# Kernel optimization log

Hardware: AMD Instinct MI355X
Metric: run time of the kernel (lower is better)

The kernel has to match this reference:

```python
import jax, jax.numpy as jnp
import numpy as np

GX, GY = 480, 360  # grid_size
EPS = 1e-5  # BatchNorm eps


def _bn(x, g, b):
    # BatchNorm1d in training mode: batch statistics, biased variance
    m = jnp.mean(x, axis=0)
    v = jnp.var(x, axis=0)
    return (x - m) * jax.lax.rsqrt(v + EPS) * g + b


def setup_inputs() -> dict:
    key = jax.random.key(0)
    ks = jax.random.split(key, 16)
    B, N, F = 2, 200000, 9
    pt_fea = jax.random.normal(ks[0], (B, N, F), dtype=jnp.float32)
    xy_ind = jax.random.randint(ks[1], (B, N, 2), 0, 360, dtype=jnp.int64)

    def lin(k, fi, fo):
        s = 1.0 / np.sqrt(fi)
        kw, kb = jax.random.split(k)
        W = jax.random.uniform(kw, (fi, fo), jnp.float32, -s, s)
        b = jax.random.uniform(kb, (fo,), jnp.float32, -s, s)
        return W, b

    W1, b1 = lin(ks[2], F, 64)
    W2, b2 = lin(ks[3], 64, 128)
    W3, b3 = lin(ks[4], 128, 256)
    W4, b4 = lin(ks[5], 256, 64)
    return {
        "pt_fea": pt_fea, "xy_ind": xy_ind,
        "bn0_g": jnp.ones((F,)), "bn0_b": jnp.zeros((F,)),
        "W1": W1, "b1": b1, "bn1_g": jnp.ones((64,)), "bn1_b": jnp.zeros((64,)),
        "W2": W2, "b2": b2, "bn2_g": jnp.ones((128,)), "bn2_b": jnp.zeros((128,)),
        "W3": W3, "b3": b3, "bn3_g": jnp.ones((256,)), "bn3_b": jnp.zeros((256,)),
        "W4": W4, "b4": b4,
    }


def reference(pt_fea, xy_ind, bn0_g, bn0_b, W1, b1, bn1_g, bn1_b,
              W2, b2, bn2_g, bn2_b, W3, b3, bn3_g, bn3_b, W4, b4):
    B, N, F = pt_fea.shape
    P = B * N  # total points
    x = pt_fea.reshape(P, F)

    # composite voxel key = batch * GX*GY + ix * GY + iy (equivalent to
    # torch.unique over the padded [batch, ix, iy] rows)
    bidx = jnp.repeat(jnp.arange(B, dtype=xy_ind.dtype), N)
    ind = xy_ind.reshape(P, 2)
    keys = bidx * (GX * GY) + ind[:, 0] * GY + ind[:, 1]
    unq_keys, unq_inv = jnp.unique(keys, return_inverse=True, size=P, fill_value=-1)

    # per-point MLP (BN -> Lin -> BN -> ReLU -> ... )
    h = _bn(x, bn0_g, bn0_b)
    h = jax.nn.relu(_bn(h @ W1 + b1, bn1_g, bn1_b))
    h = jax.nn.relu(_bn(h @ W2 + b2, bn2_g, bn2_b))
    h = jax.nn.relu(_bn(h @ W3 + b3, bn3_g, bn3_b))
    h = h @ W4 + b4  # [P, 64]

    # scatter_mean over voxel segments
    sums = jax.ops.segment_sum(h, unq_inv, num_segments=P)
    cnt = jax.ops.segment_sum(jnp.ones((P,), h.dtype), unq_inv, num_segments=P)
    pooled = sums / jnp.maximum(cnt, 1.0)[:, None]

    # decode unique keys back to [batch, ix, iy]; padded slots have key=-1
    ub = unq_keys // (GX * GY)
    rem = unq_keys % (GX * GY)
    unq = jnp.stack([ub, rem // GY, rem % GY], axis=1).astype(jnp.int64)
    return unq, pooled
```

## Files before the change

kernel.cpp:

```cpp
#include <hip/hip_runtime.h>
#include <hip/hip_bf16.h>

#define GXGY 172800
#define GYC  360
#define NKEYS 345600
#define SCAN_NB 338
#define STATS_NBLK 256
#define SQOFF 65536

typedef short short8_t __attribute__((ext_vector_type(8)));
typedef float floatx4 __attribute__((ext_vector_type(4)));

__device__ inline float bf2f(unsigned short u) {
  union { unsigned int i; float f; } v;
  v.i = ((unsigned int)u) << 16;
  return v.f;
}
__device__ inline unsigned short f2bf(float f) {
  union { float f; unsigned int i; } v;
  v.f = f;
  unsigned int lsb = (v.i >> 16) & 1u;
  return (unsigned short)((v.i + 0x7FFFu + lsb) >> 16);
}
__device__ inline unsigned int pk2bf(float lo, float hi) {
  __hip_bfloat162 h = __float22bfloat162_rn(float2{lo, hi});
  union { __hip_bfloat162 h; unsigned int u; } c;
  c.h = h;
  return c.u;
}
__device__ inline unsigned int aff2(unsigned int pr, float a0, float c0, float a1, float c1) {
  union { unsigned int i; float f; } t0, t1;
  t0.i = pr << 16; t1.i = pr & 0xFFFF0000u;
  float v0 = fmaxf(fmaf(t0.f, a0, c0), 0.f);
  float v1 = fmaxf(fmaf(t1.f, a1, c1), 0.f);
  return pk2bf(v0, v1);
}

__global__ __launch_bounds__(1024) void k_detect(const int* __restrict__ xy, int* __restrict__ flag) {
  __shared__ int any;
  if (threadIdx.x == 0) any = 0;
  __syncthreads();
  if (xy[threadIdx.x * 2 + 1] != 0) atomicOr(&any, 1);
  __syncthreads();
  if (threadIdx.x == 0) *flag = any;
}

__device__ inline void load_xy(const int* xy, const int* flag, int p, int& ix, int& iy) {
  if (*flag) { ix = xy[(size_t)p * 2]; iy = xy[(size_t)p * 2 + 1]; }
  else       { ix = xy[(size_t)p * 4]; iy = xy[(size_t)p * 4 + 2]; }
}


__global__ __launch_bounds__(256) void k_count(const int* __restrict__ xy, const int* __restrict__ flag,
                                               int* __restrict__ counts, int P, int N) {
  int p = blockIdx.x * 256 + threadIdx.x;
  if (p >= P) return;
  int ix, iy;
  load_xy(xy, flag, p, ix, iy);
  int key = ((p >= N) ? GXGY : 0) + ix * GYC + iy;
  atomicAdd(&counts[key], 1);
}

__global__ __launch_bounds__(256) void k_scan1(const int* __restrict__ counts, int* __restrict__ prefix,
                                               int* __restrict__ blockTot) {
  __shared__ int ssum[256];
  int base = blockIdx.x * 1024;
  int f[4];
  int tsum = 0;
#pragma unroll
  for (int i = 0; i < 4; ++i) {
    int k = base + threadIdx.x * 4 + i;
    f[i] = (k < NKEYS && counts[k] > 0) ? 1 : 0;
    tsum += f[i];
  }
  ssum[threadIdx.x] = tsum;
  __syncthreads();
  for (int off = 1; off < 256; off <<= 1) {
    int v = (threadIdx.x >= off) ? ssum[threadIdx.x - off] : 0;
    __syncthreads();
    if (threadIdx.x >= off) ssum[threadIdx.x] += v;
    __syncthreads();
  }
  int run = (threadIdx.x == 0) ? 0 : ssum[threadIdx.x - 1];
#pragma unroll
  for (int i = 0; i < 4; ++i) {
    int k = base + threadIdx.x * 4 + i;
    if (k < NKEYS) prefix[k] = run;
    run += f[i];
  }
  if (threadIdx.x == 255) blockTot[blockIdx.x] = ssum[255];
}

__global__ __launch_bounds__(256) void k_scan1v(const int* __restrict__ counts, int* __restrict__ prefixS,
                                                int* __restrict__ blockTot) {
  __shared__ int ssum[256];
  int base = blockIdx.x * 1024;
  int f[4];
  int tsum = 0;
#pragma unroll
  for (int i = 0; i < 4; ++i) {
    int k = base + threadIdx.x * 4 + i;
    f[i] = (k < NKEYS) ? counts[k] : 0;
    tsum += f[i];
  }
  ssum[threadIdx.x] = tsum;
  __syncthreads();
  for (int off = 1; off < 256; off <<= 1) {
    int v = (threadIdx.x >= off) ? ssum[threadIdx.x - off] : 0;
    __syncthreads();
    if (threadIdx.x >= off) ssum[threadIdx.x] += v;
    __syncthreads();
  }
  int run = (threadIdx.x == 0) ? 0 : ssum[threadIdx.x - 1];
#pragma unroll
  for (int i = 0; i < 4; ++i) {
    int k = base + threadIdx.x * 4 + i;
    if (k < NKEYS) prefixS[k] = run;
    run += f[i];
  }
  if (threadIdx.x == 255) blockTot[blockIdx.x] = ssum[255];
}

__global__ __launch_bounds__(512) void k_scan2(const int* __restrict__ blockTot, int* __restrict__ blockOff,
                                               int* __restrict__ dU) {
  __shared__ int s[512];
  int v = (threadIdx.x < SCAN_NB) ? blockTot[threadIdx.x] : 0;
  s[threadIdx.x] = v;
  __syncthreads();
  for (int off = 1; off < 512; off <<= 1) {
    int t = (threadIdx.x >= off) ? s[threadIdx.x - off] : 0;
    __syncthreads();
    if (threadIdx.x >= off) s[threadIdx.x] += t;
    __syncthreads();
  }
  if (threadIdx.x < SCAN_NB) blockOff[threadIdx.x] = s[threadIdx.x] - v;
  if (threadIdx.x == 511) *dU = s[511];
}

__global__ __launch_bounds__(256) void k_fillunq(const int* __restrict__ counts, const int* __restrict__ prefix,
                                                 const int* __restrict__ blockOff,
                                                 const int* __restrict__ prefixS, const int* __restrict__ blockOffS,
                                                 float* __restrict__ out_unq,
                                                 int2* __restrict__ rankCS) {
  int k = blockIdx.x * 256 + threadIdx.x;
  if (k >= NKEYS) return;
  int cnt = counts[k];
  if (cnt <= 0) return;
  int r = prefix[k] + blockOff[k >> 10];
  rankCS[r] = make_int2(cnt, prefixS[k] + blockOffS[k >> 10]);
  int b = k / GXGY;
  int rem = k % GXGY;
  out_unq[(size_t)r * 3 + 0] = (float)b;
  out_unq[(size_t)r * 3 + 1] = (float)(rem / GYC);
  out_unq[(size_t)r * 3 + 2] = (float)(rem % GYC);
}

__global__ __launch_bounds__(256) void k_pad(float* __restrict__ out_unq, const int* __restrict__ dU, int P) {
  int r = blockIdx.x * 256 + threadIdx.x;
  if (r >= P) return;
  if (r >= *dU) {
    out_unq[(size_t)r * 3 + 0] = -1.f;
    out_unq[(size_t)r * 3 + 1] = 479.f;
    out_unq[(size_t)r * 3 + 2] = 359.f;
  }
}

__global__ __launch_bounds__(256) void k_sortpts(const int* __restrict__ xy, const int* __restrict__ flag,
                                                 const int* __restrict__ prefixS,
                                                 const int* __restrict__ blockOffS, int* __restrict__ cursor,
                                                 int* __restrict__ sorted, int P, int N) {
  int p = blockIdx.x * 256 + threadIdx.x;
  if (p >= P) return;
  int ix, iy;
  load_xy(xy, flag, p, ix, iy);
  int key = ((p >= N) ? GXGY : 0) + ix * GYC + iy;
  int slot = prefixS[key] + blockOffS[key >> 10] + atomicAdd(&cursor[key], 1);
  sorted[slot] = p;
}


__global__ __launch_bounds__(256) void k_stats9(const float* __restrict__ x, int P, float* __restrict__ partials) {
  float s[9] = {0}, q[9] = {0};
  for (int p = blockIdx.x * 256 + threadIdx.x; p < P; p += STATS_NBLK * 256) {
#pragma unroll
    for (int k = 0; k < 9; ++k) {
      float v = x[(size_t)p * 9 + k];
      s[k] += v;
      q[k] += v * v;
    }
  }
  __shared__ float ls[256 * 9];
#pragma unroll
  for (int k = 0; k < 9; ++k) ls[threadIdx.x * 9 + k] = s[k];
  __syncthreads();
  if (threadIdx.x < 9) {
    float acc = 0;
    for (int t = 0; t < 256; ++t) acc += ls[t * 9 + threadIdx.x];
    partials[blockIdx.x * 9 + threadIdx.x] = acc;
  }
  __syncthreads();
#pragma unroll
  for (int k = 0; k < 9; ++k) ls[threadIdx.x * 9 + k] = q[k];
  __syncthreads();
  if (threadIdx.x < 9) {
    float acc = 0;
    for (int t = 0; t < 256; ++t) acc += ls[t * 9 + threadIdx.x];
    partials[SQOFF + blockIdx.x * 9 + threadIdx.x] = acc;
  }
}

__global__ void k_finalize(const float* __restrict__ partials, const float* __restrict__ gam,
                           const float* __restrict__ bet, float* __restrict__ ac, int F, int P) {
  int f = threadIdx.x;
  if (f >= F) return;
  float s = 0.f, q = 0.f;
  for (int blk = 0; blk < STATS_NBLK; ++blk) {
    s += partials[blk * F + f];
    q += partials[SQOFF + blk * F + f];
  }
  float mean = s / (float)P;
  float var = q / (float)P - mean * mean;
  float A = gam[f] * rsqrtf(var + 1e-5f);
  ac[f] = A;
  ac[256 + f] = bet[f] - mean * A;
}

__global__ void k_finalize_at(const float* __restrict__ stats, const float* __restrict__ gam,
                              const float* __restrict__ bet, float* __restrict__ ac, int F, int P) {
  int f = threadIdx.x;
  if (f >= F) return;
  float mean = stats[f] / (float)P;
  float var = stats[256 + f] / (float)P - mean * mean;
  float A = gam[f] * rsqrtf(var + 1e-5f);
  ac[f] = A;
  ac[256 + f] = bet[f] - mean * A;
}

__global__ __launch_bounds__(256) void k_stage1s(const float* __restrict__ x, const float* __restrict__ ac,
                                                 const float* __restrict__ W1, const float* __restrict__ b1,
                                                 unsigned short* __restrict__ y1, float* __restrict__ stats,
                                                 int P) {
  __shared__ float sW[576];
  __shared__ float sb[64];
  __shared__ float sa[9], sc[9];
  __shared__ float rS[256], rQ[256];
  for (int i = threadIdx.x; i < 576; i += 256) sW[i] = W1[i];
  if (threadIdx.x < 64) sb[threadIdx.x] = b1[threadIdx.x];
  if (threadIdx.x < 9) {
    sa[threadIdx.x] = ac[threadIdx.x];
    sc[threadIdx.x] = ac[256 + threadIdx.x];
  }
  __syncthreads();
  int j = threadIdx.x & 63, g = threadIdx.x >> 6;
  float sS = 0.f, sQ = 0.f;
  for (int p = blockIdx.x * 4 + g; p < P; p += gridDim.x * 4) {
    float acc = sb[j];
#pragma unroll
    for (int k = 0; k < 9; ++k) {
      float xn = fmaf(x[(size_t)p * 9 + k], sa[k], sc[k]);
      acc = fmaf(xn, sW[k * 64 + j], acc);
    }
    y1[(size_t)p * 64 + j] = (unsigned short)(pk2bf(acc, acc) & 0xFFFFu);
    sS += acc;
    sQ += acc * acc;
  }
  rS[threadIdx.x] = sS;
  rQ[threadIdx.x] = sQ;
  __syncthreads();
  if (g == 0) {
    float S = rS[j] + rS[64 + j] + rS[128 + j] + rS[192 + j];
    float Q = rQ[j] + rQ[64 + j] + rQ[128 + j] + rQ[192 + j];
    atomicAdd(&stats[j], S);
    atomicAdd(&stats[256 + j], Q);
  }
}

template <int K>
__global__ __launch_bounds__(256, 4) void k_gemmM(const unsigned short* __restrict__ X,
                                                  const float* __restrict__ acIn,
                                                  const float* __restrict__ W, const float* __restrict__ bias,
                                                  unsigned short* __restrict__ Y, float* __restrict__ stats,
                                                  int N, int P) {
  constexpr int SEGS = K / 8;
  constexpr int NIT = K / 32;
  constexpr int KPA = K + 8;
  constexpr int OFF_C = 64 * KPA * 2;
  constexpr int OFF_AC = OFF_C + 64 * 136 * 2;
  constexpr int OFF_B = OFF_AC + 512 * 4;
  constexpr int SMEM = OFF_B + 128 * 4;
  static_assert(64 * KPA * 2 + 64 * 136 * 2 >= 128 * KPA * 2, "WTtmp alias fits in A+Csm");
  __shared__ __align__(16) char smem[SMEM];
  unsigned short* A   = (unsigned short*)smem;
  unsigned short* Csm = (unsigned short*)(smem + OFF_C);
  unsigned short* WTt = (unsigned short*)smem;
  float* acL = (float*)(smem + OFF_AC);
  float* bL  = (float*)(smem + OFF_B);

  const int tid = threadIdx.x;
  const int nq = blockIdx.y;

  for (int i = tid; i < 128 * K; i += 256) {
    int k = i >> 7, n = i & 127;
    WTt[n * KPA + k] = f2bf(W[(size_t)k * N + nq * 128 + n]);
  }
  for (int i = tid; i < 512; i += 256) acL[i] = acIn[i];
  if (tid < 128) bL[tid] = bias[nq * 128 + tid];
  __syncthreads();

  const int lane = tid & 63;
  const int w = tid >> 6;
  const int li = lane & 15, lg = lane >> 4;
  const int cb = 32 * w;

  short8_t bfr[2][K / 32];
#pragma unroll
  for (int t = 0; t < 2; ++t)
#pragma unroll
    for (int s = 0; s < K / 32; ++s)
      bfr[t][s] = *(const short8_t*)&WTt[(cb + 16 * t + li) * KPA + 32 * s + 8 * lg];
  __syncthreads();

  const int tiles = P >> 6;
  float sS[2] = {0.f, 0.f}, sQ[2] = {0.f, 0.f};
  uint4 pre[NIT];
  int tile = blockIdx.x;
  if (tile < tiles) {
#pragma unroll
    for (int it = 0; it < NIT; ++it) {
      int i = tid + it * 256;
      int row = i / SEGS, seg = i % SEGS;
      pre[it] = *(const uint4*)&X[((size_t)tile * 64 + row) * K + seg * 8];
    }
  }
  for (; tile < tiles; tile += gridDim.x) {
    const size_t row0 = (size_t)tile * 64;
#pragma unroll
    for (int it = 0; it < NIT; ++it) {
      int i = tid + it * 256;
      int row = i / SEGS, seg = i % SEGS;
      const float* ap = &acL[seg * 8];
      const float* cp = &acL[256 + seg * 8];
      uint4 o;
      o.x = aff2(pre[it].x, ap[0], cp[0], ap[1], cp[1]);
      o.y = aff2(pre[it].y, ap[2], cp[2], ap[3], cp[3]);
      o.z = aff2(pre[it].z, ap[4], cp[4], ap[5], cp[5]);
      o.w = aff2(pre[it].w, ap[6], cp[6], ap[7], cp[7]);
      *(uint4*)&A[row * KPA + seg * 8] = o;
    }
    __syncthreads();
    int nt = tile + gridDim.x;
    if (nt < tiles) {
#pragma unroll
      for (int it = 0; it < NIT; ++it) {
        int i = tid + it * 256;
        int row = i / SEGS, seg = i % SEGS;
        pre[it] = *(const uint4*)&X[((size_t)nt * 64 + row) * K + seg * 8];
      }
    }

    floatx4 acc[4][2];
#pragma unroll
    for (int m = 0; m < 4; ++m)
#pragma unroll
      for (int t = 0; t < 2; ++t) acc[m][t] = (floatx4){0.f, 0.f, 0.f, 0.f};

#pragma unroll
    for (int s = 0; s < K / 32; ++s) {
      const int ko = 32 * s + 8 * lg;
      short8_t af0 = *(const short8_t*)&A[(li) * KPA + ko];
      short8_t af1 = *(const short8_t*)&A[(16 + li) * KPA + ko];
      short8_t af2 = *(const short8_t*)&A[(32 + li) * KPA + ko];
      short8_t af3 = *(const short8_t*)&A[(48 + li) * KPA + ko];
      acc[0][0] = __builtin_amdgcn_mfma_f32_16x16x32_bf16(af0, bfr[0][s], acc[0][0], 0, 0, 0);
      acc[1][0] = __builtin_amdgcn_mfma_f32_16x16x32_bf16(af1, bfr[0][s], acc[1][0], 0, 0, 0);
      acc[2][0] = __builtin_amdgcn_mfma_f32_16x16x32_bf16(af2, bfr[0][s], acc[2][0], 0, 0, 0);
      acc[3][0] = __builtin_amdgcn_mfma_f32_16x16x32_bf16(af3, bfr[0][s], acc[3][0], 0, 0, 0);
      acc[0][1] = __builtin_amdgcn_mfma_f32_16x16x32_bf16(af0, bfr[1][s], acc[0][1], 0, 0, 0);
      acc[1][1] = __builtin_amdgcn_mfma_f32_16x16x32_bf16(af1, bfr[1][s], acc[1][1], 0, 0, 0);
      acc[2][1] = __builtin_amdgcn_mfma_f32_16x16x32_bf16(af2, bfr[1][s], acc[2][1], 0, 0, 0);
      acc[3][1] = __builtin_amdgcn_mfma_f32_16x16x32_bf16(af3, bfr[1][s], acc[3][1], 0, 0, 0);
    }

#pragma unroll
    for (int m = 0; m < 4; ++m)
#pragma unroll
      for (int t = 0; t < 2; ++t) {
        int col = cb + 16 * t + li;
        float bb = bL[col];
#pragma unroll
        for (int rp = 0; rp < 2; ++rp) {
          int rowc = 16 * m + 4 * lg + 2 * rp;
          float v0 = acc[m][t][2 * rp] + bb;
          float v1 = acc[m][t][2 * rp + 1] + bb;
          unsigned int u = pk2bf(v0, v1);
          Csm[rowc * 136 + col] = (unsigned short)(u & 0xFFFFu);
          Csm[(rowc + 1) * 136 + col] = (unsigned short)(u >> 16);
          sS[t] += v0 + v1;
          sQ[t] += v0 * v0 + v1 * v1;
        }
      }
    __syncthreads();
    for (int i = tid; i < 1024; i += 256) {
      int rowc = i >> 4, seg = i & 15;
      *(uint4*)&Y[(row0 + rowc) * N + nq * 128 + seg * 8] = *(const uint4*)&Csm[rowc * 136 + seg * 8];
    }
  }

#pragma unroll
  for (int t = 0; t < 2; ++t) {
    float s = sS[t];
    s += __shfl_xor(s, 16);
    s += __shfl_xor(s, 32);
    float q = sQ[t];
    q += __shfl_xor(q, 16);
    q += __shfl_xor(q, 32);
    if (lane < 16) {
      int col = nq * 128 + cb + 16 * t + li;
      atomicAdd(&stats[col], s);
      atomicAdd(&stats[256 + col], q);
    }
  }
}

__global__ __launch_bounds__(512, 4) void k_gemm3w(const unsigned short* __restrict__ X,
                                                   const float* __restrict__ acIn,
                                                   const float* __restrict__ W, const float* __restrict__ bias,
                                                   unsigned short* __restrict__ Y, float* __restrict__ stats,
                                                   int P) {
  __shared__ __align__(16) char smem[17408 + 33792 + 2048 + 1024];
  unsigned short* A   = (unsigned short*)smem;
  unsigned short* Csm = (unsigned short*)(smem + 17408);
  float* acL = (float*)(smem + 17408 + 33792);
  float* bL  = (float*)(smem + 17408 + 33792 + 2048);

  const int tid = threadIdx.x;
  for (int i = tid; i < 512; i += 512) acL[i] = acIn[i];
  if (tid < 256) bL[tid] = bias[tid];

  const int lane = tid & 63;
  const int w = tid >> 6;
  const int li = lane & 15, lg = lane >> 4;
  const int cb = 32 * w;

  short8_t bfr[2][4];
#pragma unroll
  for (int t = 0; t < 2; ++t)
#pragma unroll
    for (int s = 0; s < 4; ++s) {
      int col = cb + 16 * t + li;
      int kb = 32 * s + 8 * lg;
      unsigned short tmp[8];
#pragma unroll
      for (int j = 0; j < 8; ++j) tmp[j] = f2bf(W[(size_t)(kb + j) * 256 + col]);
      bfr[t][s] = *(const short8_t*)tmp;
    }
  __syncthreads();

  const int tiles = P >> 6;
  float sS[2] = {0.f, 0.f}, sQ[2] = {0.f, 0.f};
  uint4 pre[2];
  int tile = blockIdx.x;
  if (tile < tiles) {
#pragma unroll
    for (int it = 0; it < 2; ++it) {
      int i = tid + it * 512;
      int row = i >> 4, seg = i & 15;
      pre[it] = *(const uint4*)&X[((size_t)tile * 64 + row) * 128 + seg * 8];
    }
  }
  for (; tile < tiles; tile += gridDim.x) {
    const size_t row0 = (size_t)tile * 64;
#pragma unroll
    for (int it = 0; it < 2; ++it) {
      int i = tid + it * 512;
      int row = i >> 4, seg = i & 15;
      const float* ap = &acL[seg * 8];
      const float* cp = &acL[256 + seg * 8];
      uint4 o;
      o.x = aff2(pre[it].x, ap[0], cp[0], ap[1], cp[1]);
      o.y = aff2(pre[it].y, ap[2], cp[2], ap[3], cp[3]);
      o.z = aff2(pre[it].z, ap[4], cp[4], ap[5], cp[5]);
      o.w = aff2(pre[it].w, ap[6], cp[6], ap[7], cp[7]);
      *(uint4*)&A[row * 136 + seg * 8] = o;
    }
    __syncthreads();
    int nt = tile + gridDim.x;
    if (nt < tiles) {
#pragma unroll
      for (int it = 0; it < 2; ++it) {
        int i = tid + it * 512;
        int row = i >> 4, seg = i & 15;
        pre[it] = *(const uint4*)&X[((size_t)nt * 64 + row) * 128 + seg * 8];
      }
    }

    floatx4 acc[4][2];
#pragma unroll
    for (int m = 0; m < 4; ++m)
#pragma unroll
      for (int t = 0; t < 2; ++t) acc[m][t] = (floatx4){0.f, 0.f, 0.f, 0.f};

#pragma unroll
    for (int s = 0; s < 4; ++s) {
      const int ko = 32 * s + 8 * lg;
      short8_t af0 = *(const short8_t*)&A[(li) * 136 + ko];
      short8_t af1 = *(const short8_t*)&A[(16 + li) * 136 + ko];
      short8_t af2 = *(const short8_t*)&A[(32 + li) * 136 + ko];
      short8_t af3 = *(const short8_t*)&A[(48 + li) * 136 + ko];
      acc[0][0] = __builtin_amdgcn_mfma_f32_16x16x32_bf16(af0, bfr[0][s], acc[0][0], 0, 0, 0);
      acc[1][0] = __builtin_amdgcn_mfma_f32_16x16x32_bf16(af1, bfr[0][s], acc[1][0], 0, 0, 0);
      acc[2][0] = __builtin_amdgcn_mfma_f32_16x16x32_bf16(af2, bfr[0][s], acc[2][0], 0, 0, 0);
      acc[3][0] = __builtin_amdgcn_mfma_f32_16x16x32_bf16(af3, bfr[0][s], acc[3][0], 0, 0, 0);
      acc[0][1] = __builtin_amdgcn_mfma_f32_16x16x32_bf16(af0, bfr[1][s], acc[0][1], 0, 0, 0);
      acc[1][1] = __builtin_amdgcn_mfma_f32_16x16x32_bf16(af1, bfr[1][s], acc[1][1], 0, 0, 0);
      acc[2][1] = __builtin_amdgcn_mfma_f32_16x16x32_bf16(af2, bfr[1][s], acc[2][1], 0, 0, 0);
      acc[3][1] = __builtin_amdgcn_mfma_f32_16x16x32_bf16(af3, bfr[1][s], acc[3][1], 0, 0, 0);
    }

#pragma unroll
    for (int m = 0; m < 4; ++m)
#pragma unroll
      for (int t = 0; t < 2; ++t) {
        int col = cb + 16 * t + li;
        float bb = bL[col];
#pragma unroll
        for (int rp = 0; rp < 2; ++rp) {
          int rowc = 16 * m + 4 * lg + 2 * rp;
          float v0 = acc[m][t][2 * rp] + bb;
          float v1 = acc[m][t][2 * rp + 1] + bb;
          unsigned int u = pk2bf(v0, v1);
          Csm[rowc * 264 + col] = (unsigned short)(u & 0xFFFFu);
          Csm[(rowc + 1) * 264 + col] = (unsigned short)(u >> 16);
          sS[t] += v0 + v1;
          sQ[t] += v0 * v0 + v1 * v1;
        }
      }
    __syncthreads();
    for (int i = tid; i < 2048; i += 512) {
      int rowc = i >> 5, seg = i & 31;
      *(uint4*)&Y[(row0 + rowc) * 256 + seg * 8] = *(const uint4*)&Csm[rowc * 264 + seg * 8];
    }
  }

#pragma unroll
  for (int t = 0; t < 2; ++t) {
    float s = sS[t];
    s += __shfl_xor(s, 16);
    s += __shfl_xor(s, 32);
    float q = sQ[t];
    q += __shfl_xor(q, 16);
    q += __shfl_xor(q, 32);
    if (lane < 16) {
      int col = cb + 16 * t + li;
      atomicAdd(&stats[col], s);
      atomicAdd(&stats[256 + col], q);
    }
  }
}

__global__ __launch_bounds__(256, 4) void k_gemm4(const unsigned short* __restrict__ y3,
                                                  const float* __restrict__ ac3,
                                                  const float* __restrict__ W4, const float* __restrict__ b4,
                                                  const int* __restrict__ sorted,
                                                  unsigned short* __restrict__ h4, int P) {
  __shared__ __align__(16) char smem[34816 + 2048 + 256 + 256];
  unsigned short* A0 = (unsigned short*)smem;
  unsigned short* A1 = (unsigned short*)(smem + 17408);
  unsigned short* WTt = (unsigned short*)smem;
  float* acL = (float*)(smem + 34816);
  float* bL  = (float*)(smem + 34816 + 2048);
  int* sIdsL = (int*)(smem + 34816 + 2048 + 256);

  const int tid = threadIdx.x;
  for (int i = tid; i < 64 * 256; i += 256) {
    int k = i >> 6, n = i & 63;
    WTt[n * 264 + k] = f2bf(W4[(size_t)k * 64 + n]);
  }
  for (int i = tid; i < 512; i += 256) acL[i] = ac3[i];
  if (tid < 64) bL[tid] = b4[tid];
  __syncthreads();

  const int lane = tid & 63;
  const int w = tid >> 6;
  const int li = lane & 15, lg = lane >> 4;
  const int cb = 16 * w;
  const int tiles = P >> 6;

  short8_t bfr[8];
#pragma unroll
  for (int s = 0; s < 8; ++s)
    bfr[s] = *(const short8_t*)&WTt[(cb + li) * 264 + 32 * s + 8 * lg];
  __syncthreads();

  int tb = blockIdx.x;
  if (tb >= tiles) return;
  if (tid < 64) sIdsL[tid] = sorted[tb * 64 + tid];
  __syncthreads();

  uint4 preA[4], preB[4];
#pragma unroll
  for (int it = 0; it < 4; ++it) {
    int i = tid + it * 256;
    int row = i >> 4, seg = i & 15;
    preA[it] = *(const uint4*)&y3[(size_t)sIdsL[row] * 256 + seg * 8];
  }

  for (; tb < tiles; tb += gridDim.x) {
    int nt = tb + gridDim.x;
    int sNext = 0;
    if (tid < 64 && nt < tiles) sNext = sorted[nt * 64 + tid];

#pragma unroll
    for (int it = 0; it < 4; ++it) {
      int i = tid + it * 256;
      int row = i >> 4, seg = i & 15;
      const float* ap = &acL[seg * 8];
      const float* cp = &acL[256 + seg * 8];
      uint4 o;
      o.x = aff2(preA[it].x, ap[0], cp[0], ap[1], cp[1]);
      o.y = aff2(preA[it].y, ap[2], cp[2], ap[3], cp[3]);
      o.z = aff2(preA[it].z, ap[4], cp[4], ap[5], cp[5]);
      o.w = aff2(preA[it].w, ap[6], cp[6], ap[7], cp[7]);
      *(uint4*)&A0[row * 136 + seg * 8] = o;
    }
    __syncthreads();

#pragma unroll
    for (int it = 0; it < 4; ++it) {
      int i = tid + it * 256;
      int row = i >> 4, seg = i & 15;
      preB[it] = *(const uint4*)&y3[(size_t)sIdsL[row] * 256 + 128 + seg * 8];
    }

    floatx4 acc[4];
#pragma unroll
    for (int m = 0; m < 4; ++m) acc[m] = (floatx4){0.f, 0.f, 0.f, 0.f};

#pragma unroll
    for (int s = 0; s < 4; ++s) {
      const int ko = 32 * s + 8 * lg;
      short8_t af0 = *(const short8_t*)&A0[(li) * 136 + ko];
      short8_t af1 = *(const short8_t*)&A0[(16 + li) * 136 + ko];
      short8_t af2 = *(const short8_t*)&A0[(32 + li) * 136 + ko];
      short8_t af3 = *(const short8_t*)&A0[(48 + li) * 136 + ko];
      acc[0] = __builtin_amdgcn_mfma_f32_16x16x32_bf16(af0, bfr[s], acc[0], 0, 0, 0);
      acc[1] = __builtin_amdgcn_mfma_f32_16x16x32_bf16(af1, bfr[s], acc[1], 0, 0, 0);
      acc[2] = __builtin_amdgcn_mfma_f32_16x16x32_bf16(af2, bfr[s], acc[2], 0, 0, 0);
      acc[3] = __builtin_amdgcn_mfma_f32_16x16x32_bf16(af3, bfr[s], acc[3], 0, 0, 0);
    }
    __syncthreads();

    if (tid < 64 && nt < tiles) sIdsL[tid] = sNext;
#pragma unroll
    for (int it = 0; it < 4; ++it) {
      int i = tid + it * 256;
      int row = i >> 4, seg = i & 15;
      const float* ap = &acL[128 + seg * 8];
      const float* cp = &acL[256 + 128 + seg * 8];
      uint4 o;
      o.x = aff2(preB[it].x, ap[0], cp[0], ap[1], cp[1]);
      o.y = aff2(preB[it].y, ap[2], cp[2], ap[3], cp[3]);
      o.z = aff2(preB[it].z, ap[4], cp[4], ap[5], cp[5]);
      o.w = aff2(preB[it].w, ap[6], cp[6], ap[7], cp[7]);
      *(uint4*)&A1[row * 136 + seg * 8] = o;
    }
    __syncthreads();

    if (nt < tiles) {
#pragma unroll
      for (int it = 0; it < 4; ++it) {
        int i = tid + it * 256;
        int row = i >> 4, seg = i & 15;
        preA[it] = *(const uint4*)&y3[(size_t)sIdsL[row] * 256 + seg * 8];
      }
    }

#pragma unroll
    for (int s = 0; s < 4; ++s) {
      const int ko = 32 * s + 8 * lg;
      short8_t af0 = *(const short8_t*)&A1[(li) * 136 + ko];
      short8_t af1 = *(const short8_t*)&A1[(16 + li) * 136 + ko];
      short8_t af2 = *(const short8_t*)&A1[(32 + li) * 136 + ko];
      short8_t af3 = *(const short8_t*)&A1[(48 + li) * 136 + ko];
      acc[0] = __builtin_amdgcn_mfma_f32_16x16x32_bf16(af0, bfr[4 + s], acc[0], 0, 0, 0);
      acc[1] = __builtin_amdgcn_mfma_f32_16x16x32_bf16(af1, bfr[4 + s], acc[1], 0, 0, 0);
      acc[2] = __builtin_amdgcn_mfma_f32_16x16x32_bf16(af2, bfr[4 + s], acc[2], 0, 0, 0);
      acc[3] = __builtin_amdgcn_mfma_f32_16x16x32_bf16(af3, bfr[4 + s], acc[3], 0, 0, 0);
    }
    __syncthreads();

    unsigned short* Csm = A1;
    {
      int col = cb + li;
      float bb = bL[col];
#pragma unroll
      for (int m = 0; m < 4; ++m)
#pragma unroll
        for (int rp = 0; rp < 2; ++rp) {
          int rowc = 16 * m + 4 * lg + 2 * rp;
          unsigned int u = pk2bf(acc[m][2 * rp] + bb, acc[m][2 * rp + 1] + bb);
          Csm[rowc * 72 + col] = (unsigned short)(u & 0xFFFFu);
          Csm[(rowc + 1) * 72 + col] = (unsigned short)(u >> 16);
        }
    }
    __syncthreads();
    for (int i = tid; i < 512; i += 256) {
      int rowc = i >> 3, seg = i & 7;
      *(uint4*)&h4[(size_t)(tb * 64 + rowc) * 64 + seg * 8] = *(const uint4*)&Csm[rowc * 72 + seg * 8];
    }
  }
}

__global__ __launch_bounds__(256) void k_gather(const unsigned short* __restrict__ h4,
                                                const int2* __restrict__ rankCS,
                                                float* __restrict__ outp, int P) {
  int wv = threadIdx.x >> 6;
  int j = threadIdx.x & 63;
  int r0 = blockIdx.x * 32 + wv * 8;
  if (r0 >= P) return;
  int cnt[8], st[8];
  int maxc = 0;
#pragma unroll
  for (int i = 0; i < 8; ++i) {
    int2 cs = (r0 + i < P) ? rankCS[r0 + i] : make_int2(0, 0);
    cnt[i] = cs.x;
    st[i] = cs.y;
    maxc = max(maxc, cs.x);
  }
  float acc[8] = {};
  for (int k = 0; k < maxc; ++k) {
#pragma unroll
    for (int i = 0; i < 8; ++i)
      if (k < cnt[i]) acc[i] += bf2f(h4[(size_t)(st[i] + k) * 64 + j]);
  }
#pragma unroll
  for (int i = 0; i < 8; ++i)
    if (r0 + i < P) outp[(size_t)(r0 + i) * 64 + j] = (cnt[i] > 0) ? acc[i] / (float)cnt[i] : 0.f;
}


extern "C" void kernel_launch(void* const* d_in, const int* in_sizes, int n_in,
                              void* d_out, int out_size, void* d_ws, size_t ws_size,
                              hipStream_t stream) {
  const float* pt_fea = (const float*)d_in[0];
  const int*   xy     = (const int*)d_in[1];
  const float* bn0_g = (const float*)d_in[2];
  const float* bn0_b = (const float*)d_in[3];
  const float* W1 = (const float*)d_in[4];
  const float* b1 = (const float*)d_in[5];
  const float* bn1_g = (const float*)d_in[6];
  const float* bn1_b = (const float*)d_in[7];
  const float* W2 = (const float*)d_in[8];
  const float* b2 = (const float*)d_in[9];
  const float* bn2_g = (const float*)d_in[10];
  const float* bn2_b = (const float*)d_in[11];
  const float* W3 = (const float*)d_in[12];
  const float* b3 = (const float*)d_in[13];
  const float* bn3_g = (const float*)d_in[14];
  const float* bn3_b = (const float*)d_in[15];
  const float* W4 = (const float*)d_in[16];
  const float* b4 = (const float*)d_in[17];

  const int P = in_sizes[0] / 9;
  const int Nhalf = P / 2;

  char* w = (char*)d_ws;
  size_t off = 0;
  auto alloc = [&](size_t bytes) -> void* {
    off = (off + 255) & ~(size_t)255;
    void* p = w + off;
    off += bytes;
    return p;
  };
  int* counts    = (int*)alloc((size_t)NKEYS * 4);
  int* prefix    = (int*)alloc((size_t)NKEYS * 4);
  int* prefixS   = (int*)alloc((size_t)NKEYS * 4);
  int* blockTot  = (int*)alloc(512 * 4);
  int* blockOff  = (int*)alloc(512 * 4);
  int* blockTotS = (int*)alloc(512 * 4);
  int* blockOffS = (int*)alloc(512 * 4);
  int* dU        = (int*)alloc(256);
  int* dUs       = (int*)alloc(256);
  int* flag      = (int*)alloc(256);
  int2* rankCS   = (int2*)alloc((size_t)P * 8);
  int* sorted    = (int*)alloc((size_t)P * 4);
  float* partials = (float*)alloc((size_t)2 * SQOFF * 4);
  float* st1 = (float*)alloc(512 * 4);
  float* st2 = (float*)alloc(512 * 4);
  float* st3 = (float*)alloc(512 * 4);
  float* ac0 = (float*)alloc(512 * 4);
  float* ac1 = (float*)alloc(512 * 4);
  float* ac2 = (float*)alloc(512 * 4);
  float* ac3 = (float*)alloc(512 * 4);
  unsigned short* y1 = (unsigned short*)alloc((size_t)P * 64 * 2);
  unsigned short* y2 = (unsigned short*)alloc((size_t)P * 128 * 2);
  unsigned short* y3 = (unsigned short*)alloc((size_t)P * 256 * 2);
  (void)ws_size; (void)n_in; (void)out_size;

  float* out_unq = (float*)d_out;
  float* out_pooled = out_unq + (size_t)P * 3;

  const int nbP = (P + 255) / 256;

  hipMemsetAsync(counts, 0, (size_t)NKEYS * 4, stream);
  hipMemsetAsync(rankCS, 0, (size_t)P * 8, stream);
  hipMemsetAsync(st1, 0, 3 * 2048, stream);
  k_detect<<<1, 1024, 0, stream>>>(xy, flag);
  k_count<<<nbP, 256, 0, stream>>>(xy, flag, counts, P, Nhalf);
  k_scan1<<<SCAN_NB, 256, 0, stream>>>(counts, prefix, blockTot);
  k_scan2<<<1, 512, 0, stream>>>(blockTot, blockOff, dU);
  k_scan1v<<<SCAN_NB, 256, 0, stream>>>(counts, prefixS, blockTotS);
  k_scan2<<<1, 512, 0, stream>>>(blockTotS, blockOffS, dUs);
  k_fillunq<<<(NKEYS + 255) / 256, 256, 0, stream>>>(counts, prefix, blockOff, prefixS, blockOffS,
                                                     out_unq, rankCS);
  k_pad<<<nbP, 256, 0, stream>>>(out_unq, dU, P);
  hipMemsetAsync(counts, 0, (size_t)NKEYS * 4, stream);
  k_sortpts<<<nbP, 256, 0, stream>>>(xy, flag, prefixS, blockOffS, counts, sorted, P, Nhalf);

  k_stats9<<<STATS_NBLK, 256, 0, stream>>>(pt_fea, P, partials);
  k_finalize<<<1, 9, 0, stream>>>(partials, bn0_g, bn0_b, ac0, 9, P);

  k_stage1s<<<2048, 256, 0, stream>>>(pt_fea, ac0, W1, b1, y1, st1, P);
  k_finalize_at<<<1, 64, 0, stream>>>(st1, bn1_g, bn1_b, ac1, 64, P);

  k_gemmM<64><<<dim3(2048, 1), 256, 0, stream>>>(y1, ac1, W2, b2, y2, st2, 128, P);
  k_finalize_at<<<1, 128, 0, stream>>>(st2, bn2_g, bn2_b, ac2, 128, P);

  k_gemm3w<<<1024, 512, 0, stream>>>(y2, ac2, W3, b3, y3, st3, P);
  k_finalize_at<<<1, 256, 0, stream>>>(st3, bn3_g, bn3_b, ac3, 256, P);

  unsigned short* h4 = y1;
  k_gemm4<<<2048, 256, 0, stream>>>(y3, ac3, W4, b4, sorted, h4, P);

  k_gather<<<(P + 31) / 32, 256, 0, stream>>>(h4, rankCS, out_pooled, P);
}
```

Before: 424.5 us.

## Tile stage-1 MLP over 32-point tiles with coalesced loads and vector bf16 stores

Rewrites the first linear layer kernel so each block stages a 32-point tile of input features in shared memory via coalesced loads, with register prefetch of the next tile. Each thread computes 8 output channels and writes them as one 16-byte packed bf16 store instead of scalar 2-byte stores. Statistics are reduced with wave shuffles before the atomics. It assumes P is a multiple of 32 and silently drops any tail points, and it adds extra barriers per tile.

Result: faster. 403.9 us (-4.9%).

```diff
diff --git a/kernel.cpp b/kernel.cpp
--- a/kernel.cpp
+++ b/kernel.cpp
@@ -243,35 +243,82 @@
   __shared__ float sW[576];
   __shared__ float sb[64];
   __shared__ float sa[9], sc[9];
-  __shared__ float rS[256], rQ[256];
-  for (int i = threadIdx.x; i < 576; i += 256) sW[i] = W1[i];
-  if (threadIdx.x < 64) sb[threadIdx.x] = b1[threadIdx.x];
-  if (threadIdx.x < 9) {
-    sa[threadIdx.x] = ac[threadIdx.x];
-    sc[threadIdx.x] = ac[256 + threadIdx.x];
-  }
-  __syncthreads();
-  int j = threadIdx.x & 63, g = threadIdx.x >> 6;
-  float sS = 0.f, sQ = 0.f;
-  for (int p = blockIdx.x * 4 + g; p < P; p += gridDim.x * 4) {
-    float acc = sb[j];
+  __shared__ float xT[288];
+  __shared__ float gS[256], gQ[256];
+  const int tid = threadIdx.x;
+  for (int i = tid; i < 576; i += 256) sW[i] = W1[i];
+  if (tid < 64) sb[tid] = b1[tid];
+  if (tid < 9) {
+    sa[tid] = ac[tid];
+    sc[tid] = ac[256 + tid];
+  }
+  const int row_l = tid >> 3;
+  const int cg = tid & 7;
+  const int tiles = P >> 5;
+  float sS[8] = {}, sQ[8] = {};
+  float pre0 = 0.f, pre1 = 0.f;
+  int tile = blockIdx.x;
+  if (tile < tiles) {
+    size_t base = (size_t)tile * 288;
+    pre0 = x[base + tid];
+    if (tid < 32) pre1 = x[base + 256 + tid];
+  }
+  __syncthreads();
+  for (; tile < tiles; tile += gridDim.x) {
+    xT[tid] = pre0;
+    if (tid < 32) xT[256 + tid] = pre1;
+    __syncthreads();
+    int nt = tile + gridDim.x;
+    if (nt < tiles) {
+      size_t base = (size_t)nt * 288;
+      pre0 = x[base + tid];
+      if (tid < 32) pre1 = x[base + 256 + tid];
+    }
+    float acc[8];
+#pragma unroll
+    for (int c = 0; c < 8; ++c) acc[c] = sb[cg * 8 + c];
 #pragma unroll
     for (int k = 0; k < 9; ++k) {
-      float xn = fmaf(x[(size_t)p * 9 + k], sa[k], sc[k]);
-      acc = fmaf(xn, sW[k * 64 + j], acc);
-    }
-    y1[(size_t)p * 64 + j] = (unsigned short)(pk2bf(acc, acc) & 0xFFFFu);
-    sS += acc;
-    sQ += acc * acc;
-  }
-  rS[threadIdx.x] = sS;
-  rQ[threadIdx.x] = sQ;
-  __syncthreads();
-  if (g == 0) {
-    float S = rS[j] + rS[64 + j] + rS[128 + j] + rS[192 + j];
-    float Q = rQ[j] + rQ[64 + j] + rQ[128 + j] + rQ[192 + j];
-    atomicAdd(&stats[j], S);
-    atomicAdd(&stats[256 + j], Q);
+      float xn = fmaf(xT[row_l * 9 + k], sa[k], sc[k]);
+#pragma unroll
+      for (int c = 0; c < 8; ++c) acc[c] = fmaf(xn, sW[k * 64 + cg * 8 + c], acc[c]);
+    }
+    uint4 o;
+    o.x = pk2bf(acc[0], acc[1]);
+    o.y = pk2bf(acc[2], acc[3]);
+    o.z = pk2bf(acc[4], acc[5]);
+    o.w = pk2bf(acc[6], acc[7]);
+    *(uint4*)&y1[((size_t)tile * 32 + row_l) * 64 + cg * 8] = o;
+#pragma unroll
+    for (int c = 0; c < 8; ++c) {
+      sS[c] += acc[c];
+      sQ[c] += acc[c] * acc[c];
+    }
+    __syncthreads();
+  }
+#pragma unroll
+  for (int c = 0; c < 8; ++c) {
+    sS[c] += __shfl_xor(sS[c], 8);
+    sS[c] += __shfl_xor(sS[c], 16);
+    sS[c] += __shfl_xor(sS[c], 32);
+    sQ[c] += __shfl_xor(sQ[c], 8);
+    sQ[c] += __shfl_xor(sQ[c], 16);
+    sQ[c] += __shfl_xor(sQ[c], 32);
+  }
+  int lane = tid & 63, wv = tid >> 6;
+  if (lane < 8) {
+#pragma unroll
+    for (int c = 0; c < 8; ++c) {
+      gS[wv * 64 + lane * 8 + c] = sS[c];
+      gQ[wv * 64 + lane * 8 + c] = sQ[c];
+    }
+  }
+  __syncthreads();
+  if (tid < 64) {
+    float S = gS[tid] + gS[64 + tid] + gS[128 + tid] + gS[192 + tid];
+    float Q = gQ[tid] + gQ[64 + tid] + gQ[128 + tid] + gQ[192 + tid];
+    atomicAdd(&stats[tid], S);
+    atomicAdd(&stats[256 + tid], Q);
   }
 }
 
```
